# Optimization experiments

Hardware: AMD Instinct MI355X
Metric: run time of the kernel (lower is better)

Reference implementation:

```python
import jax, jax.numpy as jnp
import numpy as np

NEG = -1.0e9  # matches module's max_value fill for float32


def setup_inputs() -> dict:
    key0 = jax.random.key(0)
    kq, kk, kv = jax.random.split(key0, 3)
    B, H, S, D = 2, 16, 2048, 128
    return {
        "query": jax.random.normal(kq, (B, H, S, D), dtype=jnp.float32),
        "key": jax.random.normal(kk, (B, H, S, D), dtype=jnp.float32),
        "value": jax.random.normal(kv, (B, H, S, D), dtype=jnp.float32),
        "scale": jnp.ones((1,), dtype=jnp.float32),
    }


def reference(query, key, value, scale):
    # scores = (Q K^T) * learned scalar scale   [B,H,Sq,Sk]
    scores = jnp.einsum("bhqd,bhkd->bhqk", query, key) * scale[0]
    # causal mask (use_causal_mask=True): tril over last two dims
    Sq, Sk = scores.shape[-2], scores.shape[-1]
    causal = jnp.tril(jnp.ones((Sq, Sk), dtype=bool))
    scores = jnp.where(causal, scores, jnp.asarray(NEG, scores.dtype))
    weights = jax.nn.softmax(scores, axis=-1)
    # eval mode: dropout inactive
    out = jnp.einsum("bhqk,bhkd->bhqd", weights, value)
    return out
```

## Files before the change

kernel.cpp:

```cpp
#include <hip/hip_runtime.h>
#include <hip/hip_bf16.h>

#define S_LEN 2048
#define DH    128
#define NBH   32
#define NQT   32
#define KPAD  136
#define VPAD  72

typedef __attribute__((ext_vector_type(4))) float    f32x4;
typedef __attribute__((ext_vector_type(8))) _Float16 h16x8;
typedef __attribute__((ext_vector_type(4))) _Float16 h16x4;
typedef __attribute__((ext_vector_type(2))) __fp16   fp16x2;

#if __has_builtin(__builtin_amdgcn_exp2f)
#define EXP2(x) __builtin_amdgcn_exp2f(x)
#else
#define EXP2(x) exp2f(x)
#endif

static __device__ __forceinline__ unsigned pk2(float lo, float hi) {
  union { fp16x2 h; unsigned u; } u;
  u.h = __builtin_amdgcn_cvt_pkrtz(lo, hi);
  return u.u;
}

__global__ __launch_bounds__(256, 2)
void attn_fwd(const float* __restrict__ Q, const float* __restrict__ K,
              const float* __restrict__ V, const float* __restrict__ scale,
              float* __restrict__ O) {
  __shared__ short Ks[64 * KPAD];
  __shared__ short Vt[128 * VPAD];

  const int tid  = threadIdx.x;
  const int w    = tid >> 6;
  const int lane = tid & 63;
  const int quad = lane >> 4;
  const int l16  = lane & 15;

  const int bh = blockIdx.y;
  const size_t base = (size_t)bh * (S_LEN * DH);
  const float sc = scale[0] * 1.44269504088896340736f;

  const int krow = tid >> 2, kcolf = (tid & 3) * 32;
  const int vd = (tid & 31) * 4, vkb = (tid >> 5) * 4;

  int vrow[8], voff[8];
#pragma unroll
  for (int dt = 0; dt < 8; ++dt) {
    const int row = dt * 16 + l16;
    const int mm = (row ^ (row >> 4)) & 14;
    vrow[dt] = row * VPAD;
    voff[dt] = ((quad * 2) ^ mm) << 2;
  }

  f32x4 ka[8], va[8];

#pragma unroll 1
  for (int phase = 0; phase < 2; ++phase) {
    const int jq = phase ? (NQT - 1 - (int)blockIdx.x) : (int)blockIdx.x;
    const int q0 = jq * 64;
    const int nkt = jq + 1;
    const int qrow = q0 + w * 16 + l16;

    h16x8 qf[4];
    {
      const float* qp = Q + base + (size_t)qrow * DH + quad * 8;
#pragma unroll
      for (int f = 0; f < 4; ++f) {
        f32x4 a = *(const f32x4*)(qp + f * 32);
        f32x4 b = *(const f32x4*)(qp + f * 32 + 4);
        union { h16x8 v; unsigned u[4]; } t;
        t.u[0] = pk2(a[0] * sc, a[1] * sc);
        t.u[1] = pk2(a[2] * sc, a[3] * sc);
        t.u[2] = pk2(b[0] * sc, b[1] * sc);
        t.u[3] = pk2(b[2] * sc, b[3] * sc);
        qf[f] = t.v;
      }
    }

    f32x4 Oacc[8];
#pragma unroll
    for (int i = 0; i < 8; ++i) Oacc[i] = (f32x4){0.f, 0.f, 0.f, 0.f};
    float m_run = -1e30f, l_run = 0.f;

    {
      const float* kp = K + base + (size_t)krow * DH + kcolf;
#pragma unroll
      for (int q = 0; q < 8; ++q) ka[q] = *(const f32x4*)(kp + q * 4);
#pragma unroll
      for (int kk = 0; kk < 2; ++kk) {
        const float* vp = V + base + (size_t)(vkb + kk * 32) * DH + vd;
#pragma unroll
        for (int i = 0; i < 4; ++i) va[kk * 4 + i] = *(const f32x4*)(vp + i * DH);
      }
    }

#pragma unroll 1
    for (int kt = 0; kt < nkt; ++kt) {
      const int k0 = kt * 64;

#pragma unroll
      for (int q2 = 0; q2 < 4; ++q2) {
        f32x4 a = ka[2 * q2], b = ka[2 * q2 + 1];
        union { h16x8 v; unsigned u[4]; } t;
        t.u[0] = pk2(a[0], a[1]); t.u[1] = pk2(a[2], a[3]);
        t.u[2] = pk2(b[0], b[1]); t.u[3] = pk2(b[2], b[3]);
        *(h16x8*)&Ks[krow * KPAD + kcolf + q2 * 8] = t.v;
      }
#pragma unroll
      for (int kk = 0; kk < 2; ++kk) {
        const int c = (vkb + kk * 32) >> 2;
#pragma unroll
        for (int j = 0; j < 4; ++j) {
          const int row = vd + j;
          const int mm = (row ^ (row >> 4)) & 14;
          union { h16x4 v; unsigned u[2]; } t;
          t.u[0] = pk2(va[kk * 4 + 0][j], va[kk * 4 + 1][j]);
          t.u[1] = pk2(va[kk * 4 + 2][j], va[kk * 4 + 3][j]);
          *(h16x4*)&Vt[row * VPAD + ((c ^ mm) << 2)] = t.v;
        }
      }
      __syncthreads();

      if (kt + 1 < nkt) {
        const int kn = k0 + 64;
        const float* kp = K + base + (size_t)(kn + krow) * DH + kcolf;
#pragma unroll
        for (int q = 0; q < 8; ++q) ka[q] = *(const f32x4*)(kp + q * 4);
#pragma unroll
        for (int kk = 0; kk < 2; ++kk) {
          const float* vp = V + base + (size_t)(kn + vkb + kk * 32) * DH + vd;
#pragma unroll
          for (int i = 0; i < 4; ++i) va[kk * 4 + i] = *(const f32x4*)(vp + i * DH);
        }
      }

      f32x4 st[4];
#pragma unroll
      for (int t = 0; t < 4; ++t) st[t] = (f32x4){0.f, 0.f, 0.f, 0.f};
#pragma unroll
      for (int t = 0; t < 4; ++t)
#pragma unroll
        for (int f = 0; f < 4; ++f) {
          h16x8 kf = *(const h16x8*)&Ks[(t * 16 + l16) * KPAD + f * 32 + quad * 8];
          st[t] = __builtin_amdgcn_mfma_f32_16x16x32_f16(kf, qf[f], st[t], 0, 0, 0);
        }

      if (k0 + 63 > q0 + w * 16) {
#pragma unroll
        for (int t = 0; t < 4; ++t)
#pragma unroll
          for (int r = 0; r < 4; ++r)
            if (k0 + t * 16 + quad * 4 + r > qrow) st[t][r] = -1e30f;
      }

      float mt = st[0][0];
#pragma unroll
      for (int t = 0; t < 4; ++t)
#pragma unroll
        for (int r = 0; r < 4; ++r) mt = fmaxf(mt, st[t][r]);
      mt = fmaxf(mt, __shfl_xor(mt, 16));
      mt = fmaxf(mt, __shfl_xor(mt, 32));
      const float m_new = fmaxf(m_run, mt);
      float p[16], rs = 0.f;
#pragma unroll
      for (int t = 0; t < 4; ++t)
#pragma unroll
        for (int r = 0; r < 4; ++r) { p[t * 4 + r] = EXP2(st[t][r] - m_new); rs += p[t * 4 + r]; }
      rs += __shfl_xor(rs, 16);
      rs += __shfl_xor(rs, 32);
      const float alpha = EXP2(m_run - m_new);
      l_run = l_run * alpha + rs;
      m_run = m_new;

      float aO[4];
#pragma unroll
      for (int r = 0; r < 4; ++r) aO[r] = __shfl(alpha, quad * 4 + r);
#pragma unroll
      for (int dt = 0; dt < 8; ++dt)
#pragma unroll
        for (int r = 0; r < 4; ++r) Oacc[dt][r] *= aO[r];

      int pd[8];
#pragma unroll
      for (int t = 0; t < 4; ++t) {
        pd[t * 2]     = (int)pk2(p[t * 4 + 0], p[t * 4 + 1]);
        pd[t * 2 + 1] = (int)pk2(p[t * 4 + 2], p[t * 4 + 3]);
      }
#pragma unroll
      for (int h = 0; h < 2; ++h) {
        union { h16x8 v; int u[4]; } pa;
#pragma unroll
        for (int hp = 0; hp < 4; ++hp) {
          const int src = (2 * (quad & 1) + (hp >> 1)) * 16 + l16;
          const int va_ = __shfl(pd[4 * h + (hp & 1)], src);
          const int vb_ = __shfl(pd[4 * h + 2 + (hp & 1)], src);
          pa.u[hp] = (quad >= 2) ? vb_ : va_;
        }
#pragma unroll
        for (int dt = 0; dt < 8; ++dt) {
          const int off0 = vrow[dt] + (voff[dt] ^ (h << 5));
          h16x8 vf = *(const h16x8*)&Vt[off0];
          Oacc[dt] = __builtin_amdgcn_mfma_f32_16x16x32_f16(pa.v, vf, Oacc[dt], 0, 0, 0);
        }
      }
      __syncthreads();
    }

    float lO[4];
#pragma unroll
    for (int r = 0; r < 4; ++r) lO[r] = 1.0f / __shfl(l_run, quad * 4 + r);
#pragma unroll
    for (int dt = 0; dt < 8; ++dt)
#pragma unroll
      for (int r = 0; r < 4; ++r) {
        const size_t row = q0 + w * 16 + quad * 4 + r;
        O[base + row * DH + dt * 16 + l16] = Oacc[dt][r] * lO[r];
      }
  }
}

extern "C" void kernel_launch(void* const* d_in, const int* in_sizes, int n_in,
                              void* d_out, int out_size, void* d_ws, size_t ws_size,
                              hipStream_t stream) {
  const float* Q  = (const float*)d_in[0];
  const float* K  = (const float*)d_in[1];
  const float* V  = (const float*)d_in[2];
  const float* sc = (const float*)d_in[3];
  float* O = (float*)d_out;
  dim3 grid(NQT / 2, NBH);
  attn_fwd<<<grid, dim3(256), 0, stream>>>(Q, K, V, sc, O);
}
```

Before: 264.6 us.

## Process paired causal query tiles jointly sharing each K/V tile load

```diff
diff --git a/kernel.cpp b/kernel.cpp
--- a/kernel.cpp
+++ b/kernel.cpp
@@ -4,7 +4,6 @@
 #define S_LEN 2048
 #define DH    128
 #define NBH   32
-#define NQT   32
 #define KPAD  136
 #define VPAD  72
 
@@ -38,7 +37,10 @@
   const int quad = lane >> 4;
   const int l16  = lane & 15;
 
-  const int bh = blockIdx.y;
+  const int flat = (int)blockIdx.x;
+  const int jq   = (flat >> 3) & 15;
+  const int bh   = (flat & 7) | ((flat >> 7) << 3);
+
   const size_t base = (size_t)bh * (S_LEN * DH);
   const float sc = scale[0] * 1.44269504088896340736f;
 
@@ -54,160 +56,188 @@
     voff[dt] = ((quad * 2) ^ mm) << 2;
   }
 
+  const int q0A = jq * 64;
+  const int q0B = (31 - jq) * 64;
+  const int nkt = 32 - jq;
+  const int qrowA = q0A + w * 16 + l16;
+  const int qrowB = q0B + w * 16 + l16;
+
+  h16x8 qfA[4], qfB[4];
+  {
+    const float* qpA = Q + base + (size_t)qrowA * DH + quad * 8;
+    const float* qpB = Q + base + (size_t)qrowB * DH + quad * 8;
+#pragma unroll
+    for (int f = 0; f < 4; ++f) {
+      f32x4 a = *(const f32x4*)(qpA + f * 32);
+      f32x4 b = *(const f32x4*)(qpA + f * 32 + 4);
+      union { h16x8 v; unsigned u[4]; } t;
+      t.u[0] = pk2(a[0] * sc, a[1] * sc);
+      t.u[1] = pk2(a[2] * sc, a[3] * sc);
+      t.u[2] = pk2(b[0] * sc, b[1] * sc);
+      t.u[3] = pk2(b[2] * sc, b[3] * sc);
+      qfA[f] = t.v;
+      a = *(const f32x4*)(qpB + f * 32);
+      b = *(const f32x4*)(qpB + f * 32 + 4);
+      t.u[0] = pk2(a[0] * sc, a[1] * sc);
+      t.u[1] = pk2(a[2] * sc, a[3] * sc);
+      t.u[2] = pk2(b[0] * sc, b[1] * sc);
+      t.u[3] = pk2(b[2] * sc, b[3] * sc);
+      qfB[f] = t.v;
+    }
+  }
+
+  f32x4 OA[8], OB[8];
+#pragma unroll
+  for (int i = 0; i < 8; ++i) { OA[i] = (f32x4){0.f,0.f,0.f,0.f}; OB[i] = (f32x4){0.f,0.f,0.f,0.f}; }
+  float mA = -1e30f, lA = 0.f, mB = -1e30f, lB = 0.f;
+
+  auto softmax_pack = [&](f32x4* st, float& m_run, float& l_run, f32x4* Oacc, int* pd) {
+    float mt = st[0][0];
+#pragma unroll
+    for (int t = 0; t < 4; ++t)
+#pragma unroll
+      for (int r = 0; r < 4; ++r) mt = fmaxf(mt, st[t][r]);
+    mt = fmaxf(mt, __shfl_xor(mt, 16));
+    mt = fmaxf(mt, __shfl_xor(mt, 32));
+    const float m_new = fmaxf(m_run, mt);
+    float p[16], rs = 0.f;
+#pragma unroll
+    for (int t = 0; t < 4; ++t)
+#pragma unroll
+      for (int r = 0; r < 4; ++r) { p[t*4+r] = EXP2(st[t][r] - m_new); rs += p[t*4+r]; }
+    rs += __shfl_xor(rs, 16);
+    rs += __shfl_xor(rs, 32);
+    const float alpha = EXP2(m_run - m_new);
+    l_run = l_run * alpha + rs;
+    m_run = m_new;
+    float aO[4];
+#pragma unroll
+    for (int r = 0; r < 4; ++r) aO[r] = __shfl(alpha, quad * 4 + r);
+#pragma unroll
+    for (int dt = 0; dt < 8; ++dt)
+#pragma unroll
+      for (int r = 0; r < 4; ++r) Oacc[dt][r] *= aO[r];
+#pragma unroll
+    for (int t = 0; t < 4; ++t) {
+      pd[t*2]   = (int)pk2(p[t*4+0], p[t*4+1]);
+      pd[t*2+1] = (int)pk2(p[t*4+2], p[t*4+3]);
+    }
+  };
+
   f32x4 ka[8], va[8];
+  {
+    const float* kp = K + base + (size_t)krow * DH + kcolf;
+#pragma unroll
+    for (int q = 0; q < 8; ++q) ka[q] = *(const f32x4*)(kp + q * 4);
+#pragma unroll
+    for (int kk = 0; kk < 2; ++kk) {
+      const float* vp = V + base + (size_t)(vkb + kk * 32) * DH + vd;
+#pragma unroll
+      for (int i = 0; i < 4; ++i) va[kk*4+i] = *(const f32x4*)(vp + i * DH);
+    }
+  }
 
 #pragma unroll 1
-  for (int phase = 0; phase < 2; ++phase) {
-    const int jq = phase ? (NQT - 1 - (int)blockIdx.x) : (int)blockIdx.x;
-    const int q0 = jq * 64;
-    const int nkt = jq + 1;
-    const int qrow = q0 + w * 16 + l16;
-
-    h16x8 qf[4];
-    {
-      const float* qp = Q + base + (size_t)qrow * DH + quad * 8;
+  for (int kt = 0; kt < nkt; ++kt) {
+    const int k0 = kt * 64;
+
+#pragma unroll
+    for (int q2 = 0; q2 < 4; ++q2) {
+      f32x4 a = ka[2*q2], b = ka[2*q2+1];
+      union { h16x8 v; unsigned u[4]; } t;
+      t.u[0] = pk2(a[0], a[1]); t.u[1] = pk2(a[2], a[3]);
+      t.u[2] = pk2(b[0], b[1]); t.u[3] = pk2(b[2], b[3]);
+      *(h16x8*)&Ks[krow * KPAD + kcolf + q2 * 8] = t.v;
+    }
+#pragma unroll
+    for (int kk = 0; kk < 2; ++kk) {
+      const int c = (vkb + kk * 32) >> 2;
+#pragma unroll
+      for (int j = 0; j < 4; ++j) {
+        const int row = vd + j;
+        const int mm = (row ^ (row >> 4)) & 14;
+        union { h16x4 v; unsigned u[2]; } t;
+        t.u[0] = pk2(va[kk*4+0][j], va[kk*4+1][j]);
+        t.u[1] = pk2(va[kk*4+2][j], va[kk*4+3][j]);
+        *(h16x4*)&Vt[row * VPAD + ((c ^ mm) << 2)] = t.v;
+      }
+    }
+    __syncthreads();
+
+    if (kt + 1 < nkt) {
+      const int kn = k0 + 64;
+      const float* kp = K + base + (size_t)(kn + krow) * DH + kcolf;
+#pragma unroll
+      for (int q = 0; q < 8; ++q) ka[q] = *(const f32x4*)(kp + q * 4);
+#pragma unroll
+      for (int kk = 0; kk < 2; ++kk) {
+        const float* vp = V + base + (size_t)(kn + vkb + kk * 32) * DH + vd;
+#pragma unroll
+        for (int i = 0; i < 4; ++i) va[kk*4+i] = *(const f32x4*)(vp + i * DH);
+      }
+    }
+
+    const bool actA = (kt <= jq);
+
+    f32x4 stA[4], stB[4];
+#pragma unroll
+    for (int t = 0; t < 4; ++t) { stA[t] = (f32x4){0.f,0.f,0.f,0.f}; stB[t] = (f32x4){0.f,0.f,0.f,0.f}; }
+#pragma unroll
+    for (int t = 0; t < 4; ++t)
 #pragma unroll
       for (int f = 0; f < 4; ++f) {
-        f32x4 a = *(const f32x4*)(qp + f * 32);
-        f32x4 b = *(const f32x4*)(qp + f * 32 + 4);
-        union { h16x8 v; unsigned u[4]; } t;
-        t.u[0] = pk2(a[0] * sc, a[1] * sc);
-        t.u[1] = pk2(a[2] * sc, a[3] * sc);
-        t.u[2] = pk2(b[0] * sc, b[1] * sc);
-        t.u[3] = pk2(b[2] * sc, b[3] * sc);
-        qf[f] = t.v;
-      }
-    }
-
-    f32x4 Oacc[8];
-#pragma unroll
-    for (int i = 0; i < 8; ++i) Oacc[i] = (f32x4){0.f, 0.f, 0.f, 0.f};
-    float m_run = -1e30f, l_run = 0.f;
-
-    {
-      const float* kp = K + base + (size_t)krow * DH + kcolf;
-#pragma unroll
-      for (int q = 0; q < 8; ++q) ka[q] = *(const f32x4*)(kp + q * 4);
-#pragma unroll
-      for (int kk = 0; kk < 2; ++kk) {
-        const float* vp = V + base + (size_t)(vkb + kk * 32) * DH + vd;
-#pragma unroll
-        for (int i = 0; i < 4; ++i) va[kk * 4 + i] = *(const f32x4*)(vp + i * DH);
-      }
-    }
-
-#pragma unroll 1
-    for (int kt = 0; kt < nkt; ++kt) {
-      const int k0 = kt * 64;
-
-#pragma unroll
-      for (int q2 = 0; q2 < 4; ++q2) {
-        f32x4 a = ka[2 * q2], b = ka[2 * q2 + 1];
-        union { h16x8 v; unsigned u[4]; } t;
-        t.u[0] = pk2(a[0], a[1]); t.u[1] = pk2(a[2], a[3]);
-        t.u[2] = pk2(b[0], b[1]); t.u[3] = pk2(b[2], b[3]);
-        *(h16x8*)&Ks[krow * KPAD + kcolf + q2 * 8] = t.v;
-      }
-#pragma unroll
-      for (int kk = 0; kk < 2; ++kk) {
-        const int c = (vkb + kk * 32) >> 2;
-#pragma unroll
-        for (int j = 0; j < 4; ++j) {
-          const int row = vd + j;
-          const int mm = (row ^ (row >> 4)) & 14;
-          union { h16x4 v; unsigned u[2]; } t;
-          t.u[0] = pk2(va[kk * 4 + 0][j], va[kk * 4 + 1][j]);
-          t.u[1] = pk2(va[kk * 4 + 2][j], va[kk * 4 + 3][j]);
-          *(h16x4*)&Vt[row * VPAD + ((c ^ mm) << 2)] = t.v;
+        h16x8 kf = *(const h16x8*)&Ks[(t * 16 + l16) * KPAD + f * 32 + quad * 8];
+        stB[t] = __builtin_amdgcn_mfma_f32_16x16x32_f16(kf, qfB[f], stB[t], 0, 0, 0);
+        if (actA) stA[t] = __builtin_amdgcn_mfma_f32_16x16x32_f16(kf, qfA[f], stA[t], 0, 0, 0);
+      }
+
+    if (kt == nkt - 1) {
+#pragma unroll
+      for (int t = 0; t < 4; ++t)
+#pragma unroll
+        for (int r = 0; r < 4; ++r)
+          if (k0 + t * 16 + quad * 4 + r > qrowB) stB[t][r] = -1e30f;
+    }
+    int pdA[8], pdB[8];
+    softmax_pack(stB, mB, lB, OB, pdB);
+    if (actA) {
+      if (kt == jq) {
+#pragma unroll
+        for (int t = 0; t < 4; ++t)
+#pragma unroll
+          for (int r = 0; r < 4; ++r)
+            if (k0 + t * 16 + quad * 4 + r > qrowA) stA[t][r] = -1e30f;
+      }
+      softmax_pack(stA, mA, lA, OA, pdA);
+    }
+
+#pragma unroll
+    for (int h = 0; h < 2; ++h) {
+      union { h16x8 v; int u[4]; } paA, paB;
+#pragma unroll
+      for (int hp = 0; hp < 4; ++hp) {
+        const int src = (2 * (quad & 1) + (hp >> 1)) * 16 + l16;
+        int va_ = __shfl(pdB[4*h + (hp & 1)], src);
+        int vb_ = __shfl(pdB[4*h + 2 + (hp & 1)], src);
+        paB.u[hp] = (quad >= 2) ? vb_ : va_;
+        if (actA) {
+          va_ = __shfl(pdA[4*h + (hp & 1)], src);
+          vb_ = __shfl(pdA[4*h + 2 + (hp & 1)], src);
+          paA.u[hp] = (quad >= 2) ? vb_ : va_;
         }
       }
-      __syncthreads();
-
-      if (kt + 1 < nkt) {
-        const int kn = k0 + 64;
-        const float* kp = K + base + (size_t)(kn + krow) * DH + kcolf;
-#pragma unroll
-        for (int q = 0; q < 8; ++q) ka[q] = *(const f32x4*)(kp + q * 4);
-#pragma unroll
-        for (int kk = 0; kk < 2; ++kk) {
-          const float* vp = V + base + (size_t)(kn + vkb + kk * 32) * DH + vd;
-#pragma unroll
-          for (int i = 0; i < 4; ++i) va[kk * 4 + i] = *(const f32x4*)(vp + i * DH);
-        }
-      }
-
-      f32x4 st[4];
-#pragma unroll
-      for (int t = 0; t < 4; ++t) st[t] = (f32x4){0.f, 0.f, 0.f, 0.f};
-#pragma unroll
-      for (int t = 0; t < 4; ++t)
-#pragma unroll
-        for (int f = 0; f < 4; ++f) {
-          h16x8 kf = *(const h16x8*)&Ks[(t * 16 + l16) * KPAD + f * 32 + quad * 8];
-          st[t] = __builtin_amdgcn_mfma_f32_16x16x32_f16(kf, qf[f], st[t], 0, 0, 0);
-        }
-
-      if (k0 + 63 > q0 + w * 16) {
-#pragma unroll
-        for (int t = 0; t < 4; ++t)
-#pragma unroll
-          for (int r = 0; r < 4; ++r)
-            if (k0 + t * 16 + quad * 4 + r > qrow) st[t][r] = -1e30f;
-      }
-
-      float mt = st[0][0];
-#pragma unroll
-      for (int t = 0; t < 4; ++t)
-#pragma unroll
-        for (int r = 0; r < 4; ++r) mt = fmaxf(mt, st[t][r]);
-      mt = fmaxf(mt, __shfl_xor(mt, 16));
-      mt = fmaxf(mt, __shfl_xor(mt, 32));
-      const float m_new = fmaxf(m_run, mt);
-      float p[16], rs = 0.f;
-#pragma unroll
-      for (int t = 0; t < 4; ++t)
-#pragma unroll
-        for (int r = 0; r < 4; ++r) { p[t * 4 + r] = EXP2(st[t][r] - m_new); rs += p[t * 4 + r]; }
-      rs += __shfl_xor(rs, 16);
-      rs += __shfl_xor(rs, 32);
-      const float alpha = EXP2(m_run - m_new);
-      l_run = l_run * alpha + rs;
-      m_run = m_new;
-
-      float aO[4];
-#pragma unroll
-      for (int r = 0; r < 4; ++r) aO[r] = __shfl(alpha, quad * 4 + r);
-#pragma unroll
-      for (int dt = 0; dt < 8; ++dt)
-#pragma unroll
-        for (int r = 0; r < 4; ++r) Oacc[dt][r] *= aO[r];
-
-      int pd[8];
-#pragma unroll
-      for (int t = 0; t < 4; ++t) {
-        pd[t * 2]     = (int)pk2(p[t * 4 + 0], p[t * 4 + 1]);
-        pd[t * 2 + 1] = (int)pk2(p[t * 4 + 2], p[t * 4 + 3]);
-      }
-#pragma unroll
-      for (int h = 0; h < 2; ++h) {
-        union { h16x8 v; int u[4]; } pa;
-#pragma unroll
-        for (int hp = 0; hp < 4; ++hp) {
-          const int src = (2 * (quad & 1) + (hp >> 1)) * 16 + l16;
-          const int va_ = __shfl(pd[4 * h + (hp & 1)], src);
-          const int vb_ = __shfl(pd[4 * h + 2 + (hp & 1)], src);
-          pa.u[hp] = (quad >= 2) ? vb_ : va_;
-        }
-#pragma unroll
-        for (int dt = 0; dt < 8; ++dt) {
-          const int off0 = vrow[dt] + (voff[dt] ^ (h << 5));
-          h16x8 vf = *(const h16x8*)&Vt[off0];
-          Oacc[dt] = __builtin_amdgcn_mfma_f32_16x16x32_f16(pa.v, vf, Oacc[dt], 0, 0, 0);
-        }
-      }
-      __syncthreads();
-    }
-
+#pragma unroll
+      for (int dt = 0; dt < 8; ++dt) {
+        const int off0 = vrow[dt] + (voff[dt] ^ (h << 5));
+        h16x8 vf = *(const h16x8*)&Vt[off0];
+        OB[dt] = __builtin_amdgcn_mfma_f32_16x16x32_f16(paB.v, vf, OB[dt], 0, 0, 0);
+        if (actA) OA[dt] = __builtin_amdgcn_mfma_f32_16x16x32_f16(paA.v, vf, OA[dt], 0, 0, 0);
+      }
+    }
+    __syncthreads();
+  }
+
+  auto store_o = [&](f32x4* Oacc, float l_run, int q0) {
     float lO[4];
 #pragma unroll
     for (int r = 0; r < 4; ++r) lO[r] = 1.0f / __shfl(l_run, quad * 4 + r);
@@ -218,7 +248,9 @@
         const size_t row = q0 + w * 16 + quad * 4 + r;
         O[base + row * DH + dt * 16 + l16] = Oacc[dt][r] * lO[r];
       }
-  }
+  };
+  store_o(OB, lB, q0B);
+  store_o(OA, lA, q0A);
 }
 
 extern "C" void kernel_launch(void* const* d_in, const int* in_sizes, int n_in,
@@ -229,6 +261,5 @@
   const float* V  = (const float*)d_in[2];
   const float* sc = (const float*)d_in[3];
   float* O = (float*)d_out;
-  dim3 grid(NQT / 2, NBH);
-  attn_fwd<<<grid, dim3(256), 0, stream>>>(Q, K, V, sc, O);
+  attn_fwd<<<dim3(512), dim3(256), 0, stream>>>(Q, K, V, sc, O);
 }
```

Result: faster. 246.7 us (-6.8%).
